# Performance work log

Hardware: AMD Instinct MI355X
Metric: run time of the kernel (lower is better)

The kernel has to match this reference:

```python
import jax, jax.numpy as jnp
import numpy as np

S, O, J, B = 16, 8, 32, 4096
HID, OUT_HID = 240, 512
P1, P2 = 0.5, 0.65  # Bayesian (concrete) dropout probabilities, mid of [0.5, 0.8]


def setup_inputs() -> dict:
    key = jax.random.key(0)
    ks = jax.random.split(key, 20)
    sc = 0.05
    return {
        "y_t": jax.random.normal(ks[0], (B, O), jnp.float32),
        "x_filtered_prev": jax.random.normal(ks[1], (B, S), jnp.float32),
        "F": jax.random.normal(ks[2], (S, S), jnp.float32) * sc,
        "H": jax.random.normal(ks[3], (O, S), jnp.float32) * sc,
        "W_fc_in": jax.random.normal(ks[4], (HID, 2 * S + 2 * O), jnp.float32) * sc,
        "b_fc_in": jax.random.normal(ks[5], (HID,), jnp.float32) * sc,
        "W_ih": jax.random.normal(ks[6], (3 * HID, HID), jnp.float32) * sc,
        "W_hh": jax.random.normal(ks[7], (3 * HID, HID), jnp.float32) * sc,
        "b_ih": jax.random.normal(ks[8], (3 * HID,), jnp.float32) * sc,
        "b_hh": jax.random.normal(ks[9], (3 * HID,), jnp.float32) * sc,
        "W_out1": jax.random.normal(ks[10], (OUT_HID, HID), jnp.float32) * sc,
        "b_out1": jax.random.normal(ks[11], (OUT_HID,), jnp.float32) * sc,
        "W_out2": jax.random.normal(ks[12], (S * O, OUT_HID), jnp.float32) * sc,
        "b_out2": jax.random.normal(ks[13], (S * O,), jnp.float32) * sc,
        "h_init": jax.random.normal(ks[14], (HID,), jnp.float32),
        "u1": jax.random.uniform(ks[15], (J, B, HID), jnp.float32),
        "u2": jax.random.uniform(ks[16], (J, B, OUT_HID), jnp.float32),
    }


def reference(y_t, x_filtered_prev, F, H, W_fc_in, b_fc_in, W_ih, W_hh, b_ih,
              b_hh, W_out1, b_out1, W_out2, b_out2, h_init, u1, u2):
    # --- first step of step_StateBayesianKalmanNet, fully batched over (J, B) ---
    x_pred = x_filtered_prev @ F.T                 # f(x): [B,S]
    y_pred = x_pred @ H.T                          # h(x): [B,O]
    state_inno = x_filtered_prev - x_pred          # x_filt_prev - x_pred_prev
    innovation = y_t - y_pred
    diff_state = jnp.zeros_like(x_filtered_prev)   # first step: x_prev - x_prev_prev = 0
    diff_obs = y_t - y_pred                        # y_prev = h(x_pred) on first step

    feats = jnp.concatenate([state_inno, innovation, diff_state, diff_obs], -1)  # [B,48]
    x_in = jax.nn.relu(feats @ W_fc_in.T + b_fc_in)                              # [B,HID]
    mask1 = (u1 > P1).astype(x_in.dtype) / (1.0 - P1)                            # [J,B,HID]
    x_in = x_in[None] * mask1                                                    # Bayesian dropout sample j

    # single GRU cell step (torch gate order r,z,n), h_prev = h_init broadcast
    gx = x_in @ W_ih.T + b_ih                                                    # [J,B,3H]
    gh = h_init @ W_hh.T + b_hh                                                  # [3H]
    xr, xz, xn = jnp.split(gx, 3, axis=-1)
    hr, hz, hn = jnp.split(gh, 3, axis=-1)
    r = jax.nn.sigmoid(xr + hr)
    z = jax.nn.sigmoid(xz + hz)
    n = jnp.tanh(xn + r * hn)
    h_new = (1.0 - z) * n + z * h_init                                           # [J,B,HID]

    o1 = jax.nn.relu(h_new @ W_out1.T + b_out1)                                  # [J,B,OUT_HID]
    mask2 = (u2 > P2).astype(o1.dtype) / (1.0 - P2)
    o1 = o1 * mask2
    K_vec = o1 @ W_out2.T + b_out2                                               # [J,B,S*O]
    K = K_vec.reshape(J, B, S, O)

    correction = jnp.einsum('jbso,bo->jbs', K, innovation)
    x_filt = x_pred[None] + correction                                           # [J,B,S]
    ensemble = jnp.transpose(x_filt, (1, 0, 2))                                  # [B,J,S]
    final_x = ensemble.mean(axis=1)
    final_P_diag = ensemble.var(axis=1, ddof=1)                                  # torch unbiased var

    # concrete-dropout regularization (entropy of the two dropout gates, mean over J)
    reg = -(P1 * jnp.log(P1) + (1 - P1) * jnp.log(1 - P1)) \
          - (P2 * jnp.log(P2) + (1 - P2) * jnp.log(1 - P2))
    reg = jnp.asarray(reg, final_x.dtype)

    return final_x, final_P_diag, reg, ensemble
```

## Files before the change

kernel.cpp:

```cpp
#include <hip/hip_runtime.h>
#include <hip/hip_bf16.h>
#include <math.h>

#define S_DIM 16
#define O_DIM 8
#define J_DIM 32
#define B_DIM 4096
#define HID 240
#define OHID 512

typedef __attribute__((ext_vector_type(8))) short bf16x8;
typedef __attribute__((ext_vector_type(4))) float f32x4;
#define MFMA16(a,b,c) __builtin_amdgcn_mfma_f32_16x16x32_bf16((a),(b),(c),0,0,0)

#define WS_XPRED   0
#define WS_INNO    (WS_XPRED + B_DIM*S_DIM)
#define WS_FEATS   (WS_INNO + B_DIM*O_DIM)
#define WS_XIN0    (WS_FEATS + B_DIM*48)
#define WS_GH      (WS_XIN0 + B_DIM*HID)
#define WS_WB_OFF  ((WS_GH + 960) * 4)

#define OUT_X      0
#define OUT_P      (B_DIM*S_DIM)
#define OUT_REG    (2*B_DIM*S_DIM)
#define OUT_ENS    (2*B_DIM*S_DIM + 1)

__global__ void k_aux(const float* __restrict__ W_ih, const float* __restrict__ W_hh,
                      const float* __restrict__ b_ih, const float* __restrict__ b_hh,
                      const float* __restrict__ h_init,
                      const float* __restrict__ W_o1, const float* __restrict__ W_o2,
                      __hip_bfloat16* __restrict__ Wihb, __hip_bfloat16* __restrict__ Wo1b,
                      __hip_bfloat16* __restrict__ Wo2b, float* __restrict__ ghb)
{
    int t = blockIdx.x * 256 + threadIdx.x;
    if (t < 768*256) {
        int n = t >> 8, k = t & 255;
        float v = (n < 720 && k < 240) ? W_ih[n*240 + k] : 0.0f;
        Wihb[t] = __float2bfloat16(v);
    } else if (t < 768*256 + 512*256) {
        int u = t - 768*256;
        int n = u >> 8, k = u & 255;
        float v = (k < 240) ? W_o1[n*240 + k] : 0.0f;
        Wo1b[u] = __float2bfloat16(v);
    } else if (t < 768*256 + 512*256 + 128*512) {
        int u = t - 768*256 - 512*256;
        Wo2b[u] = __float2bfloat16(W_o2[u]);
    }
    if (t < 720) {
        float a = b_hh[t];
        const float* wr = W_hh + t*240;
        for (int k = 0; k < 240; k++) a = fmaf(h_init[k], wr[k], a);
        if (t < 480) {
            ghb[t] = b_ih[t] + a;
        } else {
            ghb[t] = b_ih[t];
            ghb[t + 240] = a;
        }
    }
}

__global__ void k_pre_a(const float* __restrict__ y, const float* __restrict__ xprev,
                        const float* __restrict__ F, const float* __restrict__ Hm,
                        float* __restrict__ x_pred, float* __restrict__ inno,
                        float* __restrict__ feats)
{
    __shared__ float sF[256], sH[128];
    int tid = threadIdx.x;
    sF[tid] = F[tid];
    if (tid < 128) sH[tid] = Hm[tid];
    __syncthreads();
    int b = blockIdx.x * 256 + tid;
    float xf[16], xp[16], inn[8];
    #pragma unroll
    for (int s = 0; s < 16; s++) xf[s] = xprev[b*16 + s];
    #pragma unroll
    for (int s = 0; s < 16; s++) {
        float a = 0.f;
        #pragma unroll
        for (int k = 0; k < 16; k++) a = fmaf(xf[k], sF[s*16 + k], a);
        xp[s] = a;
    }
    #pragma unroll
    for (int o = 0; o < 8; o++) {
        float a = 0.f;
        #pragma unroll
        for (int k = 0; k < 16; k++) a = fmaf(xp[k], sH[o*16 + k], a);
        inn[o] = y[b*8 + o] - a;
    }
    #pragma unroll
    for (int s = 0; s < 16; s++) x_pred[b*16 + s] = xp[s];
    #pragma unroll
    for (int o = 0; o < 8; o++) inno[b*8 + o] = inn[o];
    float* fb = feats + b*48;
    #pragma unroll
    for (int s = 0; s < 16; s++) fb[s] = xf[s] - xp[s];
    #pragma unroll
    for (int o = 0; o < 8; o++) fb[16 + o] = inn[o];
    #pragma unroll
    for (int s = 0; s < 16; s++) fb[24 + s] = 0.f;
    #pragma unroll
    for (int o = 0; o < 8; o++) fb[40 + o] = inn[o];
}

__global__ void k_pre_b(const float* __restrict__ feats, const float* __restrict__ Wfc,
                        const float* __restrict__ bfc, float* __restrict__ x_in0)
{
    int t = blockIdx.x * 256 + threadIdx.x;
    int b = t / 240, h = t - b*240;
    const float* fb = feats + b*48;
    const float* wr = Wfc + h*48;
    float a = bfc[h];
    #pragma unroll
    for (int k = 0; k < 48; k += 4) {
        const float4 f4 = *(const float4*)&fb[k];
        const float4 w4 = *(const float4*)&wr[k];
        a = fmaf(f4.x, w4.x, fmaf(f4.y, w4.y, fmaf(f4.z, w4.z, fmaf(f4.w, w4.w, a))));
    }
    x_in0[t] = fmaxf(a, 0.f);
}

#define XS_STRIDE 264
#define O1_STRIDE 520

__global__ __launch_bounds__(256, 3) void k_main(
    const float* __restrict__ x_in0, const float* __restrict__ u1,
    const float* __restrict__ u2,
    const __hip_bfloat16* __restrict__ Wihb, const float* __restrict__ ghb,
    const float* __restrict__ h_init,
    const __hip_bfloat16* __restrict__ Wo1b, const float* __restrict__ b_out1,
    const __hip_bfloat16* __restrict__ Wo2b, const float* __restrict__ b_out2,
    const float* __restrict__ x_pred, const float* __restrict__ inno,
    float* __restrict__ ens)
{
    __shared__ __align__(16) char smem[53248];
    __hip_bfloat16* O1s = (__hip_bfloat16*)smem;
    __hip_bfloat16* Xs  = (__hip_bfloat16*)smem;
    __hip_bfloat16* Hs  = (__hip_bfloat16*)(smem + 33280);
    float* XPs   = (float*)(smem + 50176);
    float* InnoS = (float*)(smem + 52224);

    const int tid = threadIdx.x;
    const int j  = blockIdx.x >> 7;
    const int b0 = (blockIdx.x & 127) << 5;

    for (int idx = tid; idx < 32*240; idx += 256) {
        int i = idx / 240, h = idx - i*240;
        int b = b0 + i;
        float v = x_in0[b*240 + h];
        float u = u1[(j*B_DIM + b)*240 + h];
        Xs[i*XS_STRIDE + h] = __float2bfloat16((u > 0.5f) ? 2.0f*v : 0.0f);
    }
    for (int idx = tid; idx < 32*24; idx += 256) {
        int i = idx / 24, c = 240 + (idx - i*24);
        __hip_bfloat16 z = __float2bfloat16(0.0f);
        Xs[i*XS_STRIDE + c] = z;
        Hs[i*XS_STRIDE + c] = z;
    }
    XPs[tid]       = x_pred[(b0 + (tid >> 4))*16 + (tid & 15)];
    XPs[tid + 256] = x_pred[(b0 + ((tid + 256) >> 4))*16 + (tid & 15)];
    InnoS[tid]     = inno[(b0 + (tid >> 3))*8 + (tid & 7)];
    __syncthreads();

    const int wave = tid >> 6;
    const int l15  = tid & 15;
    const int quad = (tid >> 4) & 3;
    const f32x4 zero4 = {0.f, 0.f, 0.f, 0.f};

    {
        f32x4 accR[4][2], accZ[4][2], accN[4][2];
        #pragma unroll
        for (int it = 0; it < 4; it++)
            #pragma unroll
            for (int m = 0; m < 2; m++) { accR[it][m] = zero4; accZ[it][m] = zero4; accN[it][m] = zero4; }

        #pragma unroll
        for (int ks = 0; ks < 8; ks++) {
            const int ko = ks*32 + quad*8;
            bf16x8 a0 = *(const bf16x8*)&Xs[l15*XS_STRIDE + ko];
            bf16x8 a1 = *(const bf16x8*)&Xs[(16 + l15)*XS_STRIDE + ko];
            #pragma unroll
            for (int it = 0; it < 4; it++) {
                const int n = (wave + 4*it)*16 + l15;
                bf16x8 br = *(const bf16x8*)&Wihb[n*256 + ko];
                bf16x8 bz = *(const bf16x8*)&Wihb[(n + 240)*256 + ko];
                bf16x8 bn = *(const bf16x8*)&Wihb[(n + 480)*256 + ko];
                accR[it][0] = MFMA16(a0, br, accR[it][0]);
                accR[it][1] = MFMA16(a1, br, accR[it][1]);
                accZ[it][0] = MFMA16(a0, bz, accZ[it][0]);
                accZ[it][1] = MFMA16(a1, bz, accZ[it][1]);
                accN[it][0] = MFMA16(a0, bn, accN[it][0]);
                accN[it][1] = MFMA16(a1, bn, accN[it][1]);
            }
        }
        #pragma unroll
        for (int it = 0; it < 4; it++) {
            const int t = wave + 4*it;
            if (t < 15) {
                const int h = t*16 + l15;
                const float add_r = ghb[h],       add_z = ghb[240 + h];
                const float add_n = ghb[480 + h], mul_n = ghb[720 + h];
                const float hi = h_init[h];
                #pragma unroll
                for (int m = 0; m < 2; m++)
                    #pragma unroll
                    for (int r = 0; r < 4; r++) {
                        const int row = m*16 + quad*4 + r;
                        float rg = 1.0f/(1.0f + expf(-(accR[it][m][r] + add_r)));
                        float zg = 1.0f/(1.0f + expf(-(accZ[it][m][r] + add_z)));
                        float ng = tanhf(accN[it][m][r] + add_n + rg*mul_n);
                        Hs[row*XS_STRIDE + h] = __float2bfloat16((1.0f - zg)*ng + zg*hi);
                    }
            }
        }
    }
    __syncthreads();

    {
        f32x4 acc2[8][2];
        #pragma unroll
        for (int it = 0; it < 8; it++) { acc2[it][0] = zero4; acc2[it][1] = zero4; }

        #pragma unroll
        for (int ks = 0; ks < 8; ks++) {
            const int ko = ks*32 + quad*8;
            bf16x8 a0 = *(const bf16x8*)&Hs[l15*XS_STRIDE + ko];
            bf16x8 a1 = *(const bf16x8*)&Hs[(16 + l15)*XS_STRIDE + ko];
            #pragma unroll
            for (int it = 0; it < 8; it++) {
                const int n = (wave*8 + it)*16 + l15;
                bf16x8 b = *(const bf16x8*)&Wo1b[n*256 + ko];
                acc2[it][0] = MFMA16(a0, b, acc2[it][0]);
                acc2[it][1] = MFMA16(a1, b, acc2[it][1]);
            }
        }
        const float inv35 = 1.0f/0.35f;
        #pragma unroll
        for (int it = 0; it < 8; it++) {
            const int n = (wave*8 + it)*16 + l15;
            const float bb = b_out1[n];
            #pragma unroll
            for (int m = 0; m < 2; m++)
                #pragma unroll
                for (int r = 0; r < 4; r++) {
                    const int row = m*16 + quad*4 + r;
                    const int b = b0 + row;
                    float uu = u2[((j*B_DIM + b) << 9) + n];
                    float o = fmaxf(acc2[it][m][r] + bb, 0.0f);
                    o = (uu > 0.65f) ? o*inv35 : 0.0f;
                    O1s[row*O1_STRIDE + n] = __float2bfloat16(o);
                }
        }
    }
    __syncthreads();

    {
        f32x4 acc3[2][2];
        #pragma unroll
        for (int it = 0; it < 2; it++) {
            const int n = (wave*2 + it)*16 + l15;
            const float bo = b_out2[n];
            f32x4 v = {bo, bo, bo, bo};
            acc3[it][0] = v; acc3[it][1] = v;
        }
        #pragma unroll
        for (int ks = 0; ks < 16; ks++) {
            const int ko = ks*32 + quad*8;
            bf16x8 a0 = *(const bf16x8*)&O1s[l15*O1_STRIDE + ko];
            bf16x8 a1 = *(const bf16x8*)&O1s[(16 + l15)*O1_STRIDE + ko];
            #pragma unroll
            for (int it = 0; it < 2; it++) {
                const int n = (wave*2 + it)*16 + l15;
                bf16x8 b = *(const bf16x8*)&Wo2b[n*512 + ko];
                acc3[it][0] = MFMA16(a0, b, acc3[it][0]);
                acc3[it][1] = MFMA16(a1, b, acc3[it][1]);
            }
        }
        #pragma unroll
        for (int it = 0; it < 2; it++) {
            const int n = (wave*2 + it)*16 + l15;
            const int s = n >> 3, o = n & 7;
            #pragma unroll
            for (int m = 0; m < 2; m++)
                #pragma unroll
                for (int r = 0; r < 4; r++) {
                    const int row = m*16 + quad*4 + r;
                    float v = acc3[it][m][r] * InnoS[row*8 + o];
                    v += __shfl_xor(v, 1);
                    v += __shfl_xor(v, 2);
                    v += __shfl_xor(v, 4);
                    if (o == 0)
                        ens[((b0 + row)*J_DIM + j)*16 + s] = XPs[row*16 + s] + v;
                }
        }
    }
}

__global__ void k_final(const float* __restrict__ ens, float* __restrict__ out)
{
    int t = blockIdx.x * 256 + threadIdx.x;
    int b = t >> 4, s = t & 15;
    float v[32];
    #pragma unroll
    for (int jj = 0; jj < 32; jj++) v[jj] = ens[(b*32 + jj)*16 + s];
    float m = 0.f;
    #pragma unroll
    for (int jj = 0; jj < 32; jj++) m += v[jj];
    m *= (1.0f/32.0f);
    float var = 0.f;
    #pragma unroll
    for (int jj = 0; jj < 32; jj++) { float d = v[jj] - m; var = fmaf(d, d, var); }
    var *= (1.0f/31.0f);
    out[OUT_X + t] = m;
    out[OUT_P + t] = var;
    if (t == 0) out[OUT_REG] = 1.3405938195945778f;
}

extern "C" void kernel_launch(void* const* d_in, const int* in_sizes, int n_in,
                              void* d_out, int out_size, void* d_ws, size_t ws_size,
                              hipStream_t stream)
{
    (void)in_sizes; (void)n_in; (void)out_size; (void)ws_size;
    const float* y_t    = (const float*)d_in[0];
    const float* xprev  = (const float*)d_in[1];
    const float* F      = (const float*)d_in[2];
    const float* Hm     = (const float*)d_in[3];
    const float* Wfc    = (const float*)d_in[4];
    const float* bfc    = (const float*)d_in[5];
    const float* W_ih   = (const float*)d_in[6];
    const float* W_hh   = (const float*)d_in[7];
    const float* b_ih   = (const float*)d_in[8];
    const float* b_hh   = (const float*)d_in[9];
    const float* W_o1   = (const float*)d_in[10];
    const float* b_o1   = (const float*)d_in[11];
    const float* W_o2   = (const float*)d_in[12];
    const float* b_o2   = (const float*)d_in[13];
    const float* h_init = (const float*)d_in[14];
    const float* u1     = (const float*)d_in[15];
    const float* u2     = (const float*)d_in[16];

    float* out = (float*)d_out;
    float* ws  = (float*)d_ws;
    float* x_pred = ws + WS_XPRED;
    float* inno   = ws + WS_INNO;
    float* feats  = ws + WS_FEATS;
    float* x_in0  = ws + WS_XIN0;
    float* ghb    = ws + WS_GH;
    __hip_bfloat16* Wihb = (__hip_bfloat16*)((char*)d_ws + WS_WB_OFF);
    __hip_bfloat16* Wo1b = Wihb + 768*256;
    __hip_bfloat16* Wo2b = Wo1b + 512*256;
    float* ens    = out + OUT_ENS;

    k_aux<<<dim3(1536), dim3(256), 0, stream>>>(W_ih, W_hh, b_ih, b_hh, h_init,
                                                W_o1, W_o2, Wihb, Wo1b, Wo2b, ghb);
    k_pre_a<<<dim3(16), dim3(256), 0, stream>>>(y_t, xprev, F, Hm, x_pred, inno, feats);
    k_pre_b<<<dim3(3840), dim3(256), 0, stream>>>(feats, Wfc, bfc, x_in0);
    k_main<<<dim3(4096), dim3(256), 0, stream>>>(x_in0, u1, u2, Wihb, ghb, h_init,
                                                 Wo1b, b_o1, Wo2b, b_o2,
                                                 x_pred, inno, ens);
    k_final<<<dim3(256), dim3(256), 0, stream>>>(ens, out);
}
```

Measured before the change: 869.8 us.

## Bit-pack dropout mask, vectorize staging loads, shrink LDS, merge aux kernels

Dropout mask u2 is now read up front with coalesced float4 loads and packed into per-row bitmasks in shared memory, replacing the strided per-element u2 reads in the epilogue. The x_in0/u1 staging uses float4 loads and 8-byte LDS stores. The GRU gate GEMM is restructured to process one column tile at a time, cutting live accumulators. LDS is shrunk by aliasing so launch bounds can target four blocks per CU. The weight-conversion and prediction kernels are merged into one launch. An extra barrier is added before O1s overwrites the aliased Xs/Hs region.

```diff
diff --git a/kernel.cpp b/kernel.cpp
--- a/kernel.cpp
+++ b/kernel.cpp
@@ -25,51 +25,51 @@
 #define OUT_REG    (2*B_DIM*S_DIM)
 #define OUT_ENS    (2*B_DIM*S_DIM + 1)
 
-__global__ void k_aux(const float* __restrict__ W_ih, const float* __restrict__ W_hh,
-                      const float* __restrict__ b_ih, const float* __restrict__ b_hh,
-                      const float* __restrict__ h_init,
-                      const float* __restrict__ W_o1, const float* __restrict__ W_o2,
-                      __hip_bfloat16* __restrict__ Wihb, __hip_bfloat16* __restrict__ Wo1b,
-                      __hip_bfloat16* __restrict__ Wo2b, float* __restrict__ ghb)
-{
-    int t = blockIdx.x * 256 + threadIdx.x;
-    if (t < 768*256) {
-        int n = t >> 8, k = t & 255;
-        float v = (n < 720 && k < 240) ? W_ih[n*240 + k] : 0.0f;
-        Wihb[t] = __float2bfloat16(v);
-    } else if (t < 768*256 + 512*256) {
-        int u = t - 768*256;
-        int n = u >> 8, k = u & 255;
-        float v = (k < 240) ? W_o1[n*240 + k] : 0.0f;
-        Wo1b[u] = __float2bfloat16(v);
-    } else if (t < 768*256 + 512*256 + 128*512) {
-        int u = t - 768*256 - 512*256;
-        Wo2b[u] = __float2bfloat16(W_o2[u]);
-    }
-    if (t < 720) {
-        float a = b_hh[t];
-        const float* wr = W_hh + t*240;
-        for (int k = 0; k < 240; k++) a = fmaf(h_init[k], wr[k], a);
-        if (t < 480) {
-            ghb[t] = b_ih[t] + a;
-        } else {
-            ghb[t] = b_ih[t];
-            ghb[t + 240] = a;
-        }
-    }
-}
-
-__global__ void k_pre_a(const float* __restrict__ y, const float* __restrict__ xprev,
-                        const float* __restrict__ F, const float* __restrict__ Hm,
-                        float* __restrict__ x_pred, float* __restrict__ inno,
-                        float* __restrict__ feats)
+__global__ void k_aux_pre(const float* __restrict__ W_ih, const float* __restrict__ W_hh,
+                          const float* __restrict__ b_ih, const float* __restrict__ b_hh,
+                          const float* __restrict__ h_init,
+                          const float* __restrict__ W_o1, const float* __restrict__ W_o2,
+                          __hip_bfloat16* __restrict__ Wihb, __hip_bfloat16* __restrict__ Wo1b,
+                          __hip_bfloat16* __restrict__ Wo2b, float* __restrict__ ghb,
+                          const float* __restrict__ y, const float* __restrict__ xprev,
+                          const float* __restrict__ F, const float* __restrict__ Hm,
+                          float* __restrict__ x_pred, float* __restrict__ inno,
+                          float* __restrict__ feats)
 {
     __shared__ float sF[256], sH[128];
-    int tid = threadIdx.x;
+    const int tid = threadIdx.x;
+    if (blockIdx.x < 1536) {
+        int t = blockIdx.x * 256 + tid;
+        if (t < 768*256) {
+            int n = t >> 8, k = t & 255;
+            float v = (n < 720 && k < 240) ? W_ih[n*240 + k] : 0.0f;
+            Wihb[t] = __float2bfloat16(v);
+        } else if (t < 768*256 + 512*256) {
+            int u = t - 768*256;
+            int n = u >> 8, k = u & 255;
+            float v = (k < 240) ? W_o1[n*240 + k] : 0.0f;
+            Wo1b[u] = __float2bfloat16(v);
+        } else if (t < 768*256 + 512*256 + 128*512) {
+            int u = t - 768*256 - 512*256;
+            Wo2b[u] = __float2bfloat16(W_o2[u]);
+        }
+        if (t < 720) {
+            float a = b_hh[t];
+            const float* wr = W_hh + t*240;
+            for (int k = 0; k < 240; k++) a = fmaf(h_init[k], wr[k], a);
+            if (t < 480) {
+                ghb[t] = b_ih[t] + a;
+            } else {
+                ghb[t] = b_ih[t];
+                ghb[t + 240] = a;
+            }
+        }
+        return;
+    }
     sF[tid] = F[tid];
     if (tid < 128) sH[tid] = Hm[tid];
     __syncthreads();
-    int b = blockIdx.x * 256 + tid;
+    int b = (blockIdx.x - 1536) * 256 + tid;
     float xf[16], xp[16], inn[8];
     #pragma unroll
     for (int s = 0; s < 16; s++) xf[s] = xprev[b*16 + s];
@@ -122,7 +122,7 @@
 #define XS_STRIDE 264
 #define O1_STRIDE 520
 
-__global__ __launch_bounds__(256, 3) void k_main(
+__global__ __launch_bounds__(256, 4) void k_main(
     const float* __restrict__ x_in0, const float* __restrict__ u1,
     const float* __restrict__ u2,
     const __hip_bfloat16* __restrict__ Wihb, const float* __restrict__ ghb,
@@ -132,33 +132,64 @@
     const float* __restrict__ x_pred, const float* __restrict__ inno,
     float* __restrict__ ens)
 {
-    __shared__ __align__(16) char smem[53248];
+    __shared__ __align__(16) char smem[38912];
+    __hip_bfloat16* Xs  = (__hip_bfloat16*)smem;
+    __hip_bfloat16* Hs  = (__hip_bfloat16*)(smem + 16896);
     __hip_bfloat16* O1s = (__hip_bfloat16*)smem;
-    __hip_bfloat16* Xs  = (__hip_bfloat16*)smem;
-    __hip_bfloat16* Hs  = (__hip_bfloat16*)(smem + 33280);
-    float* XPs   = (float*)(smem + 50176);
-    float* InnoS = (float*)(smem + 52224);
+    unsigned int* Mbits = (unsigned int*)(smem + 33792);
+    float* XPs   = (float*)(smem + 35840);
+    float* InnoS = (float*)(smem + 37888);
 
     const int tid = threadIdx.x;
     const int j  = blockIdx.x >> 7;
     const int b0 = (blockIdx.x & 127) << 5;
 
-    for (int idx = tid; idx < 32*240; idx += 256) {
-        int i = idx / 240, h = idx - i*240;
-        int b = b0 + i;
-        float v = x_in0[b*240 + h];
-        float u = u1[(j*B_DIM + b)*240 + h];
-        Xs[i*XS_STRIDE + h] = __float2bfloat16((u > 0.5f) ? 2.0f*v : 0.0f);
-    }
-    for (int idx = tid; idx < 32*24; idx += 256) {
-        int i = idx / 24, c = 240 + (idx - i*24);
-        __hip_bfloat16 z = __float2bfloat16(0.0f);
-        Xs[i*XS_STRIDE + c] = z;
-        Hs[i*XS_STRIDE + c] = z;
-    }
-    XPs[tid]       = x_pred[(b0 + (tid >> 4))*16 + (tid & 15)];
-    XPs[tid + 256] = x_pred[(b0 + ((tid + 256) >> 4))*16 + (tid & 15)];
-    InnoS[tid]     = inno[(b0 + (tid >> 3))*8 + (tid & 7)];
+    {
+        const float4* u2t = (const float4*)(u2 + ((size_t)(j*B_DIM + b0) << 9));
+        const int sh = (tid & 7) * 4;
+        #pragma unroll
+        for (int it = 0; it < 16; ++it) {
+            float4 q = u2t[tid + 256*it];
+            unsigned int nib = (q.x > 0.65f ? 1u : 0u) | (q.y > 0.65f ? 2u : 0u)
+                             | (q.z > 0.65f ? 4u : 0u) | (q.w > 0.65f ? 8u : 0u);
+            unsigned int v = nib << sh;
+            v |= __shfl_xor(v, 1);
+            v |= __shfl_xor(v, 2);
+            v |= __shfl_xor(v, 4);
+            if ((tid & 7) == 0) Mbits[(tid >> 3) + 32*it] = v;
+        }
+    }
+
+    {
+        const float4* xt = (const float4*)(x_in0 + b0*240);
+        const float4* ut = (const float4*)(u1 + (size_t)(j*B_DIM + b0)*240);
+        #pragma unroll
+        for (int it = 0; it < 8; ++it) {
+            int idx = tid + 256*it;
+            if (idx < 1920) {
+                float4 xv = xt[idx];
+                float4 uv = ut[idx];
+                int flat = idx * 4;
+                int i = flat / 240;
+                int h = flat - i*240;
+                __hip_bfloat16 o[4];
+                o[0] = __float2bfloat16(uv.x > 0.5f ? 2.0f*xv.x : 0.0f);
+                o[1] = __float2bfloat16(uv.y > 0.5f ? 2.0f*xv.y : 0.0f);
+                o[2] = __float2bfloat16(uv.z > 0.5f ? 2.0f*xv.z : 0.0f);
+                o[3] = __float2bfloat16(uv.w > 0.5f ? 2.0f*xv.w : 0.0f);
+                *(uint2*)&Xs[i*XS_STRIDE + h] = *(const uint2*)o;
+            }
+        }
+    }
+    if (tid < 128) {
+        int row = tid >> 2, c = 240 + ((tid & 3) << 2);
+        uint2 z = {0u, 0u};
+        *(uint2*)&Xs[row*XS_STRIDE + c] = z;
+        *(uint2*)&Hs[row*XS_STRIDE + c] = z;
+    }
+    XPs[tid]       = x_pred[b0*16 + tid];
+    XPs[tid + 256] = x_pred[b0*16 + tid + 256];
+    InnoS[tid]     = inno[b0*8 + tid];
     __syncthreads();
 
     const int wave = tid >> 6;
@@ -166,51 +197,45 @@
     const int quad = (tid >> 4) & 3;
     const f32x4 zero4 = {0.f, 0.f, 0.f, 0.f};
 
-    {
-        f32x4 accR[4][2], accZ[4][2], accN[4][2];
-        #pragma unroll
-        for (int it = 0; it < 4; it++)
-            #pragma unroll
-            for (int m = 0; m < 2; m++) { accR[it][m] = zero4; accZ[it][m] = zero4; accN[it][m] = zero4; }
-
-        #pragma unroll
-        for (int ks = 0; ks < 8; ks++) {
+    #pragma unroll 1
+    for (int it = 0; it < 4; ++it) {
+        f32x4 aR[2], aZ[2], aN[2];
+        #pragma unroll
+        for (int m = 0; m < 2; ++m) { aR[m] = zero4; aZ[m] = zero4; aN[m] = zero4; }
+
+        const int nrow = (wave + 4*it)*16 + l15;
+        const __hip_bfloat16* wr = Wihb + nrow*256;
+        #pragma unroll
+        for (int ks = 0; ks < 8; ++ks) {
             const int ko = ks*32 + quad*8;
             bf16x8 a0 = *(const bf16x8*)&Xs[l15*XS_STRIDE + ko];
             bf16x8 a1 = *(const bf16x8*)&Xs[(16 + l15)*XS_STRIDE + ko];
-            #pragma unroll
-            for (int it = 0; it < 4; it++) {
-                const int n = (wave + 4*it)*16 + l15;
-                bf16x8 br = *(const bf16x8*)&Wihb[n*256 + ko];
-                bf16x8 bz = *(const bf16x8*)&Wihb[(n + 240)*256 + ko];
-                bf16x8 bn = *(const bf16x8*)&Wihb[(n + 480)*256 + ko];
-                accR[it][0] = MFMA16(a0, br, accR[it][0]);
-                accR[it][1] = MFMA16(a1, br, accR[it][1]);
-                accZ[it][0] = MFMA16(a0, bz, accZ[it][0]);
-                accZ[it][1] = MFMA16(a1, bz, accZ[it][1]);
-                accN[it][0] = MFMA16(a0, bn, accN[it][0]);
-                accN[it][1] = MFMA16(a1, bn, accN[it][1]);
-            }
-        }
-        #pragma unroll
-        for (int it = 0; it < 4; it++) {
-            const int t = wave + 4*it;
-            if (t < 15) {
-                const int h = t*16 + l15;
-                const float add_r = ghb[h],       add_z = ghb[240 + h];
-                const float add_n = ghb[480 + h], mul_n = ghb[720 + h];
-                const float hi = h_init[h];
+            bf16x8 br = *(const bf16x8*)&wr[ko];
+            bf16x8 bz = *(const bf16x8*)&wr[240*256 + ko];
+            bf16x8 bn = *(const bf16x8*)&wr[480*256 + ko];
+            aR[0] = MFMA16(a0, br, aR[0]);
+            aR[1] = MFMA16(a1, br, aR[1]);
+            aZ[0] = MFMA16(a0, bz, aZ[0]);
+            aZ[1] = MFMA16(a1, bz, aZ[1]);
+            aN[0] = MFMA16(a0, bn, aN[0]);
+            aN[1] = MFMA16(a1, bn, aN[1]);
+        }
+        const int t = wave + 4*it;
+        if (t < 15) {
+            const int h = t*16 + l15;
+            const float add_r = ghb[h],       add_z = ghb[240 + h];
+            const float add_n = ghb[480 + h], mul_n = ghb[720 + h];
+            const float hi = h_init[h];
+            #pragma unroll
+            for (int m = 0; m < 2; ++m)
                 #pragma unroll
-                for (int m = 0; m < 2; m++)
-                    #pragma unroll
-                    for (int r = 0; r < 4; r++) {
-                        const int row = m*16 + quad*4 + r;
-                        float rg = 1.0f/(1.0f + expf(-(accR[it][m][r] + add_r)));
-                        float zg = 1.0f/(1.0f + expf(-(accZ[it][m][r] + add_z)));
-                        float ng = tanhf(accN[it][m][r] + add_n + rg*mul_n);
-                        Hs[row*XS_STRIDE + h] = __float2bfloat16((1.0f - zg)*ng + zg*hi);
-                    }
-            }
+                for (int r = 0; r < 4; ++r) {
+                    const int row = m*16 + quad*4 + r;
+                    float rg = 1.0f/(1.0f + expf(-(aR[m][r] + add_r)));
+                    float zg = 1.0f/(1.0f + expf(-(aZ[m][r] + add_z)));
+                    float ng = tanhf(aN[m][r] + add_n + rg*mul_n);
+                    Hs[row*XS_STRIDE + h] = __float2bfloat16((1.0f - zg)*ng + zg*hi);
+                }
         }
     }
     __syncthreads();
@@ -221,32 +246,34 @@
         for (int it = 0; it < 8; it++) { acc2[it][0] = zero4; acc2[it][1] = zero4; }
 
         #pragma unroll
-        for (int ks = 0; ks < 8; ks++) {
+        for (int ks = 0; ks < 8; ++ks) {
             const int ko = ks*32 + quad*8;
             bf16x8 a0 = *(const bf16x8*)&Hs[l15*XS_STRIDE + ko];
             bf16x8 a1 = *(const bf16x8*)&Hs[(16 + l15)*XS_STRIDE + ko];
             #pragma unroll
-            for (int it = 0; it < 8; it++) {
+            for (int it = 0; it < 8; ++it) {
                 const int n = (wave*8 + it)*16 + l15;
                 bf16x8 b = *(const bf16x8*)&Wo1b[n*256 + ko];
                 acc2[it][0] = MFMA16(a0, b, acc2[it][0]);
                 acc2[it][1] = MFMA16(a1, b, acc2[it][1]);
             }
         }
+        __syncthreads();
         const float inv35 = 1.0f/0.35f;
         #pragma unroll
-        for (int it = 0; it < 8; it++) {
+        for (int it = 0; it < 8; ++it) {
             const int n = (wave*8 + it)*16 + l15;
             const float bb = b_out1[n];
-            #pragma unroll
-            for (int m = 0; m < 2; m++)
+            const int wbase = wave*4 + (it >> 1);
+            const int bitpos = ((it & 1) << 4) | l15;
+            #pragma unroll
+            for (int m = 0; m < 2; ++m)
                 #pragma unroll
-                for (int r = 0; r < 4; r++) {
+                for (int r = 0; r < 4; ++r) {
                     const int row = m*16 + quad*4 + r;
-                    const int b = b0 + row;
-                    float uu = u2[((j*B_DIM + b) << 9) + n];
+                    unsigned int mw = Mbits[row*16 + wbase];
                     float o = fmaxf(acc2[it][m][r] + bb, 0.0f);
-                    o = (uu > 0.65f) ? o*inv35 : 0.0f;
+                    o = ((mw >> bitpos) & 1u) ? o*inv35 : 0.0f;
                     O1s[row*O1_STRIDE + n] = __float2bfloat16(o);
                 }
         }
@@ -256,19 +283,19 @@
     {
         f32x4 acc3[2][2];
         #pragma unroll
-        for (int it = 0; it < 2; it++) {
+        for (int it = 0; it < 2; ++it) {
             const int n = (wave*2 + it)*16 + l15;
             const float bo = b_out2[n];
             f32x4 v = {bo, bo, bo, bo};
             acc3[it][0] = v; acc3[it][1] = v;
         }
         #pragma unroll
-        for (int ks = 0; ks < 16; ks++) {
+        for (int ks = 0; ks < 16; ++ks) {
             const int ko = ks*32 + quad*8;
             bf16x8 a0 = *(const bf16x8*)&O1s[l15*O1_STRIDE + ko];
             bf16x8 a1 = *(const bf16x8*)&O1s[(16 + l15)*O1_STRIDE + ko];
             #pragma unroll
-            for (int it = 0; it < 2; it++) {
+            for (int it = 0; it < 2; ++it) {
                 const int n = (wave*2 + it)*16 + l15;
                 bf16x8 b = *(const bf16x8*)&Wo2b[n*512 + ko];
                 acc3[it][0] = MFMA16(a0, b, acc3[it][0]);
@@ -276,13 +303,13 @@
             }
         }
         #pragma unroll
-        for (int it = 0; it < 2; it++) {
+        for (int it = 0; it < 2; ++it) {
             const int n = (wave*2 + it)*16 + l15;
             const int s = n >> 3, o = n & 7;
             #pragma unroll
-            for (int m = 0; m < 2; m++)
+            for (int m = 0; m < 2; ++m)
                 #pragma unroll
-                for (int r = 0; r < 4; r++) {
+                for (int r = 0; r < 4; ++r) {
                     const int row = m*16 + quad*4 + r;
                     float v = acc3[it][m][r] * InnoS[row*8 + o];
                     v += __shfl_xor(v, 1);
@@ -350,9 +377,9 @@
     __hip_bfloat16* Wo2b = Wo1b + 512*256;
     float* ens    = out + OUT_ENS;
 
-    k_aux<<<dim3(1536), dim3(256), 0, stream>>>(W_ih, W_hh, b_ih, b_hh, h_init,
-                                                W_o1, W_o2, Wihb, Wo1b, Wo2b, ghb);
-    k_pre_a<<<dim3(16), dim3(256), 0, stream>>>(y_t, xprev, F, Hm, x_pred, inno, feats);
+    k_aux_pre<<<dim3(1552), dim3(256), 0, stream>>>(W_ih, W_hh, b_ih, b_hh, h_init,
+                                                    W_o1, W_o2, Wihb, Wo1b, Wo2b, ghb,
+                                                    y_t, xprev, F, Hm, x_pred, inno, feats);
     k_pre_b<<<dim3(3840), dim3(256), 0, stream>>>(feats, Wfc, bfc, x_in0);
     k_main<<<dim3(4096), dim3(256), 0, stream>>>(x_in0, u1, u2, Wihb, ghb, h_init,
                                                  Wo1b, b_o1, Wo2b, b_o2,
```

After: 843.9 us. 1.03x faster.
